# Optimization experiments

Hardware: AMD Instinct MI355X
Metric: run time of the kernel (lower is better)

Reference implementation:

```python
import jax, jax.numpy as jnp
import numpy as np

N_USER = 50000
N_ITEM = 50000
D_IN = 128
D_OUT = 128
N_EDGE = 600000


def _sage(x_src, x_dst, ei, Wl, bl, Wr):
    # PyG SAGEConv: out = lin_l(mean_{j in N(i)} x_j) + lin_r(x_i)
    # lin_l has bias, lin_r has no bias. Weights are [out, in].
    src, dst = ei[0], ei[1]
    n_dst = x_dst.shape[0]
    msg = x_src[src]                                            # [E, D_in] gather
    agg = jax.ops.segment_sum(msg, dst, num_segments=n_dst)     # [N_dst, D_in]
    cnt = jax.ops.segment_sum(jnp.ones((ei.shape[1],), x_src.dtype), dst,
                              num_segments=n_dst)
    mean = agg / jnp.maximum(cnt, 1.0)[:, None]                 # isolated nodes -> 0
    return mean @ Wl.T + bl + x_dst @ Wr.T


def setup_inputs() -> dict:
    key = jax.random.key(0)
    ks = jax.random.split(key, 16)
    inp = {
        "x_user": jax.random.normal(ks[0], (N_USER, D_IN), jnp.float32),
        "x_item": jax.random.normal(ks[1], (N_ITEM, D_IN), jnp.float32),
        "ei_rates": jax.random.randint(ks[2], (2, N_EDGE), 0, N_USER, jnp.int64 if jax.config.jax_enable_x64 else jnp.int32),
        "ei_rev": jax.random.randint(ks[3], (2, N_EDGE), 0, N_USER, jnp.int64 if jax.config.jax_enable_x64 else jnp.int32),
        "ei_follows": jax.random.randint(ks[4], (2, N_EDGE), 0, N_USER, jnp.int64 if jax.config.jax_enable_x64 else jnp.int32),
    }
    s = 1.0 / np.sqrt(D_IN)
    names = ["rates", "rev", "fol"]
    for i, nm in enumerate(names):
        inp[f"Wl_{nm}"] = jax.random.uniform(ks[5 + 3 * i], (D_OUT, D_IN), jnp.float32, -s, s)
        inp[f"bl_{nm}"] = jax.random.uniform(ks[6 + 3 * i], (D_OUT,), jnp.float32, -s, s)
        inp[f"Wr_{nm}"] = jax.random.uniform(ks[7 + 3 * i], (D_OUT, D_IN), jnp.float32, -s, s)
    return inp


def reference(x_user, x_item, ei_rates, ei_rev, ei_follows,
              Wl_rates, bl_rates, Wr_rates,
              Wl_rev, bl_rev, Wr_rev,
              Wl_fol, bl_fol, Wr_fol):
    # relation (user -rates-> item): src=user, dst=item
    out_item = _sage(x_user, x_item, ei_rates, Wl_rates, bl_rates, Wr_rates)
    # relation (item -rev_rates-> user): src=item, dst=user
    out_user_rev = _sage(x_item, x_user, ei_rev, Wl_rev, bl_rev, Wr_rev)
    # relation (user -follows-> user)
    out_user_fol = _sage(x_user, x_user, ei_follows, Wl_fol, bl_fol, Wr_fol)
    # HeteroConv aggr='mean': average relation outputs per dst node type
    out_user = (out_user_rev + out_user_fol) * 0.5
    return out_user, out_item
```

## Files before the change

### kernel.cpp

```cpp
#include <hip/hip_runtime.h>

#define D 128
#define NBB 392

typedef __attribute__((ext_vector_type(8))) short bf16x8;
typedef __attribute__((ext_vector_type(4))) float f32x4;

__device__ inline unsigned short f2bf(float f) {
  unsigned u = __builtin_bit_cast(unsigned, f);
  unsigned r = u + 0x7FFFu + ((u >> 16) & 1u);
  return (unsigned short)(r >> 16);
}
__device__ inline float bf2f(unsigned short b) {
  unsigned u = ((unsigned)b) << 16;
  return __builtin_bit_cast(float, u);
}

struct SetupArgs {
  const float* xu; const float* xi;
  unsigned short* xbu; unsigned short* xbi;
  int n4u, n4i, nbConv;
  const int* ei[3]; int ne[3]; int nbh[3]; int nbHist;
  int* bh;
  const float* Wl_rates; const float* Wr_rates; const float* bl_rates;
  const float* Wl_rev;   const float* Wr_rev;   const float* bl_rev;
  const float* Wl_fol;   const float* Wr_fol;   const float* bl_fol;
  unsigned short* Wb_user; unsigned short* Wb_item;
  float* b_user; float* b_item;
};

__global__ void __launch_bounds__(256) setup_kernel(SetupArgs S) {
  const int tid = threadIdx.x;
  int b = blockIdx.x;
  if (b < S.nbConv) {
    int i = b * 256 + tid;
    const float* x;
    unsigned short* xb;
    if (i < S.n4u) { x = S.xu; xb = S.xbu; }
    else { i -= S.n4u; if (i >= S.n4i) return; x = S.xi; xb = S.xbi; }
    float4 v = ((const float4*)x)[i];
    ushort4 o;
    o.x = f2bf(v.x); o.y = f2bf(v.y); o.z = f2bf(v.z); o.w = f2bf(v.w);
    ((ushort4*)xb)[i] = o;
    return;
  }
  b -= S.nbConv;
  if (b < S.nbHist) {
    int rel = 0;
    while (b >= S.nbh[rel]) { b -= S.nbh[rel]; rel++; }
    __shared__ int lh[NBB];
    for (int t = tid; t < NBB; t += 256) lh[t] = 0;
    __syncthreads();
    const int ne = S.ne[rel];
    const int* dsts = S.ei[rel] + ne;
    const int base = b * 2048;
#pragma unroll
    for (int k = 0; k < 8; k++) {
      int i = base + k * 256 + tid;
      if (i < ne) atomicAdd(&lh[dsts[i] >> 7], 1);
    }
    __syncthreads();
    for (int t = tid; t < NBB; t += 256)
      if (lh[t]) atomicAdd(&S.bh[rel * NBB + t], lh[t]);
    return;
  }
  b -= S.nbHist;
  int idx = b * 256 + tid;
  if (idx >= 128 * 384) return;
  int n = idx / 384, k = idx - n * 384;
  float v;
  if (k < 128)      v = 0.5f * S.Wl_rev[n * 128 + k];
  else if (k < 256) v = 0.5f * S.Wl_fol[n * 128 + (k - 128)];
  else              v = 0.5f * (S.Wr_rev[n * 128 + (k - 256)] + S.Wr_fol[n * 128 + (k - 256)]);
  S.Wb_user[n * 384 + k] = f2bf(v);
  if (k < 256) {
    float w = (k < 128) ? S.Wl_rates[n * 128 + k] : S.Wr_rates[n * 128 + (k - 128)];
    S.Wb_item[n * 256 + k] = f2bf(w);
  }
  if (idx < 128) {
    S.b_item[idx] = S.bl_rates[idx];
    S.b_user[idx] = 0.5f * (S.bl_rev[idx] + S.bl_fol[idx]);
  }
}

__global__ void __launch_bounds__(192) scanb_kernel(const int* __restrict__ bh,
                                                    int* __restrict__ bbase,
                                                    int* __restrict__ bcur, int nbkt) {
  int w = threadIdx.x >> 6, l = threadIdx.x & 63;
  if (w >= 3) return;
  const int off = w * NBB;
  int v[7];
  int s0 = 0;
#pragma unroll
  for (int k = 0; k < 7; k++) {
    int idx = l * 7 + k;
    v[k] = (idx < nbkt) ? bh[off + idx] : 0;
    s0 += v[k];
  }
  int s = s0;
  for (int dlt = 1; dlt < 64; dlt <<= 1) {
    int t = __shfl_up(s, dlt);
    if (l >= dlt) s += t;
  }
  int run = s - s0;
#pragma unroll
  for (int k = 0; k < 7; k++) {
    int idx = l * 7 + k;
    if (idx < nbkt) { bbase[off + idx] = run; bcur[off + idx] = run; run += v[k]; }
  }
  if (l == 63) bbase[off + nbkt] = run;
}

struct PArgs { const int* ei[3]; int ne[3]; int nb[3]; unsigned* part[3]; };

__global__ void __launch_bounds__(256) part_kernel(PArgs P, int* __restrict__ bcur,
                                                   int nbkt) {
  int b = blockIdx.x, rel = 0;
  while (b >= P.nb[rel]) { b -= P.nb[rel]; rel++; }
  const int ne = P.ne[rel];
  const int* src = P.ei[rel];
  const int* dst = src + ne;
  const int base = b * 4096;
  const int tn = min(4096, ne - base);
  __shared__ int lh[NBB], lscan[NBB], gb[NBB], lcur[NBB];
  __shared__ uint2 pairs[4096];
  const int tid = threadIdx.x;
  for (int t = tid; t < NBB; t += 256) lh[t] = 0;
  __syncthreads();
#pragma unroll
  for (int k = 0; k < 16; k++) {
    int i = base + k * 256 + tid;
    if (i < ne) atomicAdd(&lh[dst[i] >> 7], 1);
  }
  __syncthreads();
  if (tid < 64) {
    int v[7];
    int s0 = 0;
#pragma unroll
    for (int k = 0; k < 7; k++) {
      int idx = tid * 7 + k;
      v[k] = (idx < NBB) ? lh[idx] : 0;
      s0 += v[k];
    }
    int s = s0;
    for (int dlt = 1; dlt < 64; dlt <<= 1) {
      int t = __shfl_up(s, dlt);
      if (tid >= dlt) s += t;
    }
    int run = s - s0;
#pragma unroll
    for (int k = 0; k < 7; k++) {
      int idx = tid * 7 + k;
      if (idx < NBB) { lscan[idx] = run; run += v[k]; }
    }
  }
  __syncthreads();
  for (int t = tid; t < nbkt; t += 256) {
    gb[t] = atomicAdd(&bcur[rel * NBB + t], lh[t]);
    lcur[t] = lscan[t];
  }
  __syncthreads();
#pragma unroll
  for (int k = 0; k < 16; k++) {
    int i = base + k * 256 + tid;
    if (i < ne) {
      int d = dst[i];
      int slot = atomicAdd(&lcur[d >> 7], 1);
      pairs[slot] = (uint2){(unsigned)src[i], (unsigned)d};
    }
  }
  __syncthreads();
  unsigned* __restrict__ out = P.part[rel];
#pragma unroll
  for (int k = 0; k < 16; k++) {
    int slot = k * 256 + tid;
    if (slot < tn) {
      uint2 p = pairs[slot];
      int bin = (int)(p.y >> 7);
      out[gb[bin] + (slot - lscan[bin])] = p.x | ((p.y & 127u) << 25);
    }
  }
}

struct BAArgs {
  const unsigned* part[3];
  const unsigned short* xb[3];
  unsigned short* mean[3];
  int m[3];
};

__global__ void __launch_bounds__(256) bagg_kernel(BAArgs A, const int* __restrict__ bbase,
                                                   int nbkt) {
  const int rel = blockIdx.x / nbkt;
  const int b = blockIdx.x - rel * nbkt;
  const int bs = bbase[rel * NBB + b];
  const int be = bbase[rel * NBB + b + 1];
  const int n = be - bs;
  const unsigned* __restrict__ pp = A.part[rel] + bs;
  const unsigned short* __restrict__ x = A.xb[rel];
  unsigned short* __restrict__ mean = A.mean[rel];
  const int m = A.m[rel];
  const int tid = threadIdx.x;
  const int w = tid >> 6, lane = tid & 63;
  const size_t loff = lane * 2;
  __shared__ unsigned sorted[4096];
  __shared__ int lcnt[128], lofs[128], lcur[128];

  if (n > 4096) {
    for (int r = w; r < 128; r += 4) {
      int gdst = b * 128 + r;
      if (gdst >= m) break;
      float a0 = 0.f, a1 = 0.f;
      int cnt = 0;
      for (int j = 0; j < n; j++) {
        unsigned p = pp[j];
        if ((int)(p >> 25) == r) {
          unsigned v = *(const unsigned*)(x + (size_t)(p & 0x1FFFFFFu) * D + loff);
          a0 += bf2f((unsigned short)(v & 0xFFFFu));
          a1 += bf2f((unsigned short)(v >> 16));
          cnt++;
        }
      }
      float inv = 1.0f / (float)max(cnt, 1);
      unsigned o = (unsigned)f2bf(a0 * inv) | ((unsigned)f2bf(a1 * inv) << 16);
      *(unsigned*)(mean + (size_t)gdst * D + loff) = o;
    }
    return;
  }

  if (tid < 128) lcnt[tid] = 0;
  __syncthreads();
  for (int i = tid; i < n; i += 256) atomicAdd(&lcnt[pp[i] >> 25], 1);
  __syncthreads();
  if (tid < 64) {
    int v0 = lcnt[2 * tid], v1 = lcnt[2 * tid + 1];
    int s0 = v0 + v1, s = s0;
    for (int dlt = 1; dlt < 64; dlt <<= 1) {
      int t = __shfl_up(s, dlt);
      if (tid >= dlt) s += t;
    }
    int ex = s - s0;
    lofs[2 * tid] = ex;
    lofs[2 * tid + 1] = ex + v0;
  }
  __syncthreads();
  if (tid < 128) lcur[tid] = lofs[tid];
  __syncthreads();
  for (int i = tid; i < n; i += 256) {
    unsigned p = pp[i];
    int slot = atomicAdd(&lcur[p >> 25], 1);
    sorted[slot] = p & 0x1FFFFFFu;
  }
  __syncthreads();

  for (int r = w; r < 128; r += 8) {
    const int rA = r, rB = r + 4;
    const int gA = b * 128 + rA, gB = b * 128 + rB;
    if (gA >= m) break;
    const bool doB = gB < m;
    int jA = lofs[rA];
    const int eA = lcur[rA];
    int jB = doB ? lofs[rB] : 0;
    const int eB = doB ? lcur[rB] : 0;
    float aA0=0,aA1=0,bA0=0,bA1=0,cA0=0,cA1=0,dA0=0,dA1=0;
    float aB0=0,aB1=0,bB0=0,bB1=0,cB0=0,cB1=0,dB0=0,dB1=0;
    while (jA + 4 <= eA && jB + 4 <= eB) {
      unsigned sA0 = sorted[jA], sA1 = sorted[jA+1], sA2 = sorted[jA+2], sA3 = sorted[jA+3];
      unsigned sB0 = sorted[jB], sB1 = sorted[jB+1], sB2 = sorted[jB+2], sB3 = sorted[jB+3];
      unsigned vA0 = *(const unsigned*)(x + (size_t)sA0 * D + loff);
      unsigned vA1 = *(const unsigned*)(x + (size_t)sA1 * D + loff);
      unsigned vA2 = *(const unsigned*)(x + (size_t)sA2 * D + loff);
      unsigned vA3 = *(const unsigned*)(x + (size_t)sA3 * D + loff);
      unsigned vB0 = *(const unsigned*)(x + (size_t)sB0 * D + loff);
      unsigned vB1 = *(const unsigned*)(x + (size_t)sB1 * D + loff);
      unsigned vB2 = *(const unsigned*)(x + (size_t)sB2 * D + loff);
      unsigned vB3 = *(const unsigned*)(x + (size_t)sB3 * D + loff);
      aA0 += bf2f((unsigned short)(vA0 & 0xFFFFu)); aA1 += bf2f((unsigned short)(vA0 >> 16));
      bA0 += bf2f((unsigned short)(vA1 & 0xFFFFu)); bA1 += bf2f((unsigned short)(vA1 >> 16));
      cA0 += bf2f((unsigned short)(vA2 & 0xFFFFu)); cA1 += bf2f((unsigned short)(vA2 >> 16));
      dA0 += bf2f((unsigned short)(vA3 & 0xFFFFu)); dA1 += bf2f((unsigned short)(vA3 >> 16));
      aB0 += bf2f((unsigned short)(vB0 & 0xFFFFu)); aB1 += bf2f((unsigned short)(vB0 >> 16));
      bB0 += bf2f((unsigned short)(vB1 & 0xFFFFu)); bB1 += bf2f((unsigned short)(vB1 >> 16));
      cB0 += bf2f((unsigned short)(vB2 & 0xFFFFu)); cB1 += bf2f((unsigned short)(vB2 >> 16));
      dB0 += bf2f((unsigned short)(vB3 & 0xFFFFu)); dB1 += bf2f((unsigned short)(vB3 >> 16));
      jA += 4; jB += 4;
    }
    for (; jA + 4 <= eA; jA += 4) {
      unsigned s0 = sorted[jA], s1 = sorted[jA+1], s2 = sorted[jA+2], s3 = sorted[jA+3];
      unsigned v0 = *(const unsigned*)(x + (size_t)s0 * D + loff);
      unsigned v1 = *(const unsigned*)(x + (size_t)s1 * D + loff);
      unsigned v2 = *(const unsigned*)(x + (size_t)s2 * D + loff);
      unsigned v3 = *(const unsigned*)(x + (size_t)s3 * D + loff);
      aA0 += bf2f((unsigned short)(v0 & 0xFFFFu)); aA1 += bf2f((unsigned short)(v0 >> 16));
      bA0 += bf2f((unsigned short)(v1 & 0xFFFFu)); bA1 += bf2f((unsigned short)(v1 >> 16));
      cA0 += bf2f((unsigned short)(v2 & 0xFFFFu)); cA1 += bf2f((unsigned short)(v2 >> 16));
      dA0 += bf2f((unsigned short)(v3 & 0xFFFFu)); dA1 += bf2f((unsigned short)(v3 >> 16));
    }
    for (; jA < eA; jA++) {
      unsigned s = sorted[jA];
      unsigned v = *(const unsigned*)(x + (size_t)s * D + loff);
      aA0 += bf2f((unsigned short)(v & 0xFFFFu)); aA1 += bf2f((unsigned short)(v >> 16));
    }
    for (; jB + 4 <= eB; jB += 4) {
      unsigned s0 = sorted[jB], s1 = sorted[jB+1], s2 = sorted[jB+2], s3 = sorted[jB+3];
      unsigned v0 = *(const unsigned*)(x + (size_t)s0 * D + loff);
      unsigned v1 = *(const unsigned*)(x + (size_t)s1 * D + loff);
      unsigned v2 = *(const unsigned*)(x + (size_t)s2 * D + loff);
      unsigned v3 = *(const unsigned*)(x + (size_t)s3 * D + loff);
      aB0 += bf2f((unsigned short)(v0 & 0xFFFFu)); aB1 += bf2f((unsigned short)(v0 >> 16));
      bB0 += bf2f((unsigned short)(v1 & 0xFFFFu)); bB1 += bf2f((unsigned short)(v1 >> 16));
      cB0 += bf2f((unsigned short)(v2 & 0xFFFFu)); cB1 += bf2f((unsigned short)(v2 >> 16));
      dB0 += bf2f((unsigned short)(v3 & 0xFFFFu)); dB1 += bf2f((unsigned short)(v3 >> 16));
    }
    for (; jB < eB; jB++) {
      unsigned s = sorted[jB];
      unsigned v = *(const unsigned*)(x + (size_t)s * D + loff);
      aB0 += bf2f((unsigned short)(v & 0xFFFFu)); aB1 += bf2f((unsigned short)(v >> 16));
    }
    {
      float v0 = (aA0 + bA0) + (cA0 + dA0);
      float v1 = (aA1 + bA1) + (cA1 + dA1);
      float inv = 1.0f / (float)max(eA - lofs[rA], 1);
      unsigned o = (unsigned)f2bf(v0 * inv) | ((unsigned)f2bf(v1 * inv) << 16);
      *(unsigned*)(mean + (size_t)gA * D + loff) = o;
    }
    if (doB) {
      float v0 = (aB0 + bB0) + (cB0 + dB0);
      float v1 = (aB1 + bB1) + (cB1 + dB1);
      float inv = 1.0f / (float)max(eB - lofs[rB], 1);
      unsigned o = (unsigned)f2bf(v0 * inv) | ((unsigned)f2bf(v1 * inv) << 16);
      *(unsigned*)(mean + (size_t)gB * D + loff) = o;
    }
  }
}

struct BSrcs { const unsigned short* s[3]; };
struct GemmArgs {
  BSrcs su, si;
  const unsigned short* wbU; const unsigned short* wbI;
  const float* bU; const float* bI;
  float* outU; float* outI;
  int MU, MI, nbU;
};

__global__ void __launch_bounds__(256) gemm2_kernel(GemmArgs A) {
  const bool isU = (int)blockIdx.x < A.nbU;
  const int bid = isU ? blockIdx.x : blockIdx.x - A.nbU;
  const BSrcs S = isU ? A.su : A.si;
  const unsigned short* __restrict__ Wb = isU ? A.wbU : A.wbI;
  const int K = isU ? 384 : 256;
  const float* __restrict__ bias = isU ? A.bU : A.bI;
  float* __restrict__ out = isU ? A.outU : A.outI;
  const int M = isU ? A.MU : A.MI;

  __shared__ __align__(16) unsigned short As[128][72];
  __shared__ __align__(16) unsigned short Ws[128][72];
  const int tid = threadIdx.x;
  const int lane = tid & 63;
  const int wave = tid >> 6;
  const int wr = (wave >> 1) * 64;
  const int wc = (wave & 1) * 64;
  const int l15 = lane & 15;
  const int quad = lane >> 4;
  const int m0 = bid * 128;

  f32x4 acc[4][4];
#pragma unroll
  for (int r = 0; r < 4; r++)
#pragma unroll
    for (int c = 0; c < 4; c++) acc[r][c] = (f32x4){0.f, 0.f, 0.f, 0.f};

  const int srow = tid >> 1, shalf = tid & 1;
  const int nchunks = K >> 6;
  for (int ch = 0; ch < nchunks; ch++) {
    const unsigned short* sp = S.s[ch >> 1];
    const int coff = (ch & 1) << 6;
    {
      int mm = min(m0 + srow, M - 1);
      const uint4* g = (const uint4*)(sp + (size_t)mm * D + coff + shalf * 32);
      uint4* ld = (uint4*)(&As[srow][shalf * 32]);
      ld[0] = g[0]; ld[1] = g[1]; ld[2] = g[2]; ld[3] = g[3];
    }
    {
      const uint4* g = (const uint4*)(Wb + (size_t)srow * K + ch * 64 + shalf * 32);
      uint4* ld = (uint4*)(&Ws[srow][shalf * 32]);
      ld[0] = g[0]; ld[1] = g[1]; ld[2] = g[2]; ld[3] = g[3];
    }
    __syncthreads();
#pragma unroll
    for (int kk = 0; kk < 64; kk += 32) {
      const int kb = kk + quad * 8;
      bf16x8 a0 = *(const bf16x8*)&As[wr + l15][kb];
      bf16x8 a1 = *(const bf16x8*)&As[wr + 16 + l15][kb];
      bf16x8 a2 = *(const bf16x8*)&As[wr + 32 + l15][kb];
      bf16x8 a3 = *(const bf16x8*)&As[wr + 48 + l15][kb];
      bf16x8 b0 = *(const bf16x8*)&Ws[wc + l15][kb];
      bf16x8 b1 = *(const bf16x8*)&Ws[wc + 16 + l15][kb];
      bf16x8 b2 = *(const bf16x8*)&Ws[wc + 32 + l15][kb];
      bf16x8 b3 = *(const bf16x8*)&Ws[wc + 48 + l15][kb];
      acc[0][0] = __builtin_amdgcn_mfma_f32_16x16x32_bf16(a0, b0, acc[0][0], 0, 0, 0);
      acc[0][1] = __builtin_amdgcn_mfma_f32_16x16x32_bf16(a0, b1, acc[0][1], 0, 0, 0);
      acc[0][2] = __builtin_amdgcn_mfma_f32_16x16x32_bf16(a0, b2, acc[0][2], 0, 0, 0);
      acc[0][3] = __builtin_amdgcn_mfma_f32_16x16x32_bf16(a0, b3, acc[0][3], 0, 0, 0);
      acc[1][0] = __builtin_amdgcn_mfma_f32_16x16x32_bf16(a1, b0, acc[1][0], 0, 0, 0);
      acc[1][1] = __builtin_amdgcn_mfma_f32_16x16x32_bf16(a1, b1, acc[1][1], 0, 0, 0);
      acc[1][2] = __builtin_amdgcn_mfma_f32_16x16x32_bf16(a1, b2, acc[1][2], 0, 0, 0);
      acc[1][3] = __builtin_amdgcn_mfma_f32_16x16x32_bf16(a1, b3, acc[1][3], 0, 0, 0);
      acc[2][0] = __builtin_amdgcn_mfma_f32_16x16x32_bf16(a2, b0, acc[2][0], 0, 0, 0);
      acc[2][1] = __builtin_amdgcn_mfma_f32_16x16x32_bf16(a2, b1, acc[2][1], 0, 0, 0);
      acc[2][2] = __builtin_amdgcn_mfma_f32_16x16x32_bf16(a2, b2, acc[2][2], 0, 0, 0);
      acc[2][3] = __builtin_amdgcn_mfma_f32_16x16x32_bf16(a2, b3, acc[2][3], 0, 0, 0);
      acc[3][0] = __builtin_amdgcn_mfma_f32_16x16x32_bf16(a3, b0, acc[3][0], 0, 0, 0);
      acc[3][1] = __builtin_amdgcn_mfma_f32_16x16x32_bf16(a3, b1, acc[3][1], 0, 0, 0);
      acc[3][2] = __builtin_amdgcn_mfma_f32_16x16x32_bf16(a3, b2, acc[3][2], 0, 0, 0);
      acc[3][3] = __builtin_amdgcn_mfma_f32_16x16x32_bf16(a3, b3, acc[3][3], 0, 0, 0);
    }
    __syncthreads();
  }
#pragma unroll
  for (int c = 0; c < 4; c++) {
    const int n = wc + c * 16 + l15;
    const float bv = bias[n];
#pragma unroll
    for (int r = 0; r < 4; r++) {
      const int mrow = m0 + wr + r * 16 + quad * 4;
#pragma unroll
      for (int i = 0; i < 4; i++) {
        if (mrow + i < M) out[(size_t)(mrow + i) * D + n] = acc[r][c][i] + bv;
      }
    }
  }
}

extern "C" void kernel_launch(void* const* d_in, const int* in_sizes, int n_in,
                              void* d_out, int out_size, void* d_ws, size_t ws_size,
                              hipStream_t stream) {
  const float* x_user   = (const float*)d_in[0];
  const float* x_item   = (const float*)d_in[1];
  const int*   ei_rates = (const int*)d_in[2];
  const int*   ei_rev   = (const int*)d_in[3];
  const int*   ei_fol   = (const int*)d_in[4];
  const float* Wl_rates = (const float*)d_in[5];
  const float* bl_rates = (const float*)d_in[6];
  const float* Wr_rates = (const float*)d_in[7];
  const float* Wl_rev   = (const float*)d_in[8];
  const float* bl_rev   = (const float*)d_in[9];
  const float* Wr_rev   = (const float*)d_in[10];
  const float* Wl_fol   = (const float*)d_in[11];
  const float* bl_fol   = (const float*)d_in[12];
  const float* Wr_fol   = (const float*)d_in[13];

  const int NU = in_sizes[0] / D;
  const int NI = in_sizes[1] / D;
  const int E_rates = in_sizes[2] / 2;
  const int E_rev   = in_sizes[3] / 2;
  const int E_fol   = in_sizes[4] / 2;
  const int nbkt = ((NU > NI ? NU : NI) + 127) / 128;

  char* wsb = (char*)d_ws;
  size_t off = 0;
  auto take = [&](size_t bytes) {
    char* p = wsb + off;
    off += (bytes + 15) & ~(size_t)15;
    return p;
  };
  int* bhist = (int*)take(3 * NBB * 4);
  const size_t zero_bytes = off;
  int* bbase = (int*)take(3 * NBB * 4);
  int* bcur  = (int*)take(3 * NBB * 4);
  unsigned* part_rates = (unsigned*)take((size_t)E_rates * 4);
  unsigned* part_rev   = (unsigned*)take((size_t)E_rev * 4);
  unsigned* part_fol   = (unsigned*)take((size_t)E_fol * 4);
  unsigned short* xb_user    = (unsigned short*)take((size_t)NU * D * 2);
  unsigned short* xb_item    = (unsigned short*)take((size_t)NI * D * 2);
  unsigned short* mean_rates = (unsigned short*)take((size_t)NI * D * 2);
  unsigned short* mean_rev   = (unsigned short*)take((size_t)NU * D * 2);
  unsigned short* mean_fol   = (unsigned short*)take((size_t)NU * D * 2);
  unsigned short* Wb_user    = (unsigned short*)take(128 * 384 * 2);
  unsigned short* Wb_item    = (unsigned short*)take(128 * 256 * 2);
  float* b_user = (float*)take(128 * 4);
  float* b_item = (float*)take(128 * 4);

  hipMemsetAsync(d_ws, 0, zero_bytes, stream);

  SetupArgs SA;
  SA.xu = x_user; SA.xi = x_item; SA.xbu = xb_user; SA.xbi = xb_item;
  SA.n4u = NU * D / 4; SA.n4i = NI * D / 4;
  SA.nbConv = (SA.n4u + SA.n4i + 255) / 256;
  SA.ei[0] = ei_rates; SA.ne[0] = E_rates; SA.nbh[0] = (E_rates + 2047) / 2048;
  SA.ei[1] = ei_rev;   SA.ne[1] = E_rev;   SA.nbh[1] = (E_rev + 2047) / 2048;
  SA.ei[2] = ei_fol;   SA.ne[2] = E_fol;   SA.nbh[2] = (E_fol + 2047) / 2048;
  SA.nbHist = SA.nbh[0] + SA.nbh[1] + SA.nbh[2];
  SA.bh = bhist;
  SA.Wl_rates = Wl_rates; SA.Wr_rates = Wr_rates; SA.bl_rates = bl_rates;
  SA.Wl_rev = Wl_rev; SA.Wr_rev = Wr_rev; SA.bl_rev = bl_rev;
  SA.Wl_fol = Wl_fol; SA.Wr_fol = Wr_fol; SA.bl_fol = bl_fol;
  SA.Wb_user = Wb_user; SA.Wb_item = Wb_item;
  SA.b_user = b_user; SA.b_item = b_item;
  const int nbPrep = (128 * 384 + 255) / 256;
  setup_kernel<<<SA.nbConv + SA.nbHist + nbPrep, 256, 0, stream>>>(SA);

  scanb_kernel<<<1, 192, 0, stream>>>(bhist, bbase, bcur, nbkt);

  PArgs P;
  P.ei[0] = ei_rates; P.ne[0] = E_rates; P.nb[0] = (E_rates + 4095) / 4096; P.part[0] = part_rates;
  P.ei[1] = ei_rev;   P.ne[1] = E_rev;   P.nb[1] = (E_rev + 4095) / 4096;   P.part[1] = part_rev;
  P.ei[2] = ei_fol;   P.ne[2] = E_fol;   P.nb[2] = (E_fol + 4095) / 4096;   P.part[2] = part_fol;
  part_kernel<<<P.nb[0] + P.nb[1] + P.nb[2], 256, 0, stream>>>(P, bcur, nbkt);

  BAArgs BA;
  BA.part[0] = part_rates; BA.xb[0] = xb_user; BA.mean[0] = mean_rates; BA.m[0] = NI;
  BA.part[1] = part_rev;   BA.xb[1] = xb_item; BA.mean[1] = mean_rev;   BA.m[1] = NU;
  BA.part[2] = part_fol;   BA.xb[2] = xb_user; BA.mean[2] = mean_fol;   BA.m[2] = NU;
  bagg_kernel<<<3 * nbkt, 256, 0, stream>>>(BA, bbase, nbkt);

  GemmArgs gma;
  gma.su.s[0] = mean_rev;   gma.su.s[1] = mean_fol; gma.su.s[2] = xb_user;
  gma.si.s[0] = mean_rates; gma.si.s[1] = xb_item;  gma.si.s[2] = nullptr;
  gma.wbU = Wb_user; gma.wbI = Wb_item;
  gma.bU = b_user;   gma.bI = b_item;
  gma.outU = (float*)d_out;
  gma.outI = (float*)d_out + (size_t)NU * D;
  gma.MU = NU; gma.MI = NI;
  gma.nbU = (NU + 127) / 128;
  const int nbI = (NI + 127) / 128;
  gemm2_kernel<<<gma.nbU + nbI, 256, 0, stream>>>(gma);
}
```

Baseline: 308.1 us.

## Fuse bucketed neighbor-mean aggregation into the GEMM kernel via shared memory

Merges the bucket aggregation kernel into the MFMA GEMM kernel. Each 128-row block computes the per-relation mean directly into a shared-memory A tile and multiplies it against the matching weight slice, so the bf16 mean buffers are never written to or read back from global memory and one launch disappears. It also skips the global atomicAdd in partitioning for empty bins. The trade-off is fewer independent blocks doing gather work (user blocks now handle two relations serially), larger shared-memory use that may lower occupancy, and gather latency that is no longer overlapped with MFMA work in other blocks.

After: 350.9 us. 1.14x slower.

```diff
diff --git a/kernel.cpp b/kernel.cpp
--- a/kernel.cpp
+++ b/kernel.cpp
@@ -156,7 +156,8 @@
   }
   __syncthreads();
   for (int t = tid; t < nbkt; t += 256) {
-    gb[t] = atomicAdd(&bcur[rel * NBB + t], lh[t]);
+    int c = lh[t];
+    gb[t] = c ? atomicAdd(&bcur[rel * NBB + t], c) : 0;
     lcur[t] = lscan[t];
   }
   __syncthreads();
@@ -182,187 +183,41 @@
   }
 }
 
-struct BAArgs {
+struct FArgs {
   const unsigned* part[3];
-  const unsigned short* xb[3];
-  unsigned short* mean[3];
-  int m[3];
-};
-
-__global__ void __launch_bounds__(256) bagg_kernel(BAArgs A, const int* __restrict__ bbase,
-                                                   int nbkt) {
-  const int rel = blockIdx.x / nbkt;
-  const int b = blockIdx.x - rel * nbkt;
-  const int bs = bbase[rel * NBB + b];
-  const int be = bbase[rel * NBB + b + 1];
-  const int n = be - bs;
-  const unsigned* __restrict__ pp = A.part[rel] + bs;
-  const unsigned short* __restrict__ x = A.xb[rel];
-  unsigned short* __restrict__ mean = A.mean[rel];
-  const int m = A.m[rel];
-  const int tid = threadIdx.x;
-  const int w = tid >> 6, lane = tid & 63;
-  const size_t loff = lane * 2;
-  __shared__ unsigned sorted[4096];
-  __shared__ int lcnt[128], lofs[128], lcur[128];
-
-  if (n > 4096) {
-    for (int r = w; r < 128; r += 4) {
-      int gdst = b * 128 + r;
-      if (gdst >= m) break;
-      float a0 = 0.f, a1 = 0.f;
-      int cnt = 0;
-      for (int j = 0; j < n; j++) {
-        unsigned p = pp[j];
-        if ((int)(p >> 25) == r) {
-          unsigned v = *(const unsigned*)(x + (size_t)(p & 0x1FFFFFFu) * D + loff);
-          a0 += bf2f((unsigned short)(v & 0xFFFFu));
-          a1 += bf2f((unsigned short)(v >> 16));
-          cnt++;
-        }
-      }
-      float inv = 1.0f / (float)max(cnt, 1);
-      unsigned o = (unsigned)f2bf(a0 * inv) | ((unsigned)f2bf(a1 * inv) << 16);
-      *(unsigned*)(mean + (size_t)gdst * D + loff) = o;
-    }
-    return;
-  }
-
-  if (tid < 128) lcnt[tid] = 0;
-  __syncthreads();
-  for (int i = tid; i < n; i += 256) atomicAdd(&lcnt[pp[i] >> 25], 1);
-  __syncthreads();
-  if (tid < 64) {
-    int v0 = lcnt[2 * tid], v1 = lcnt[2 * tid + 1];
-    int s0 = v0 + v1, s = s0;
-    for (int dlt = 1; dlt < 64; dlt <<= 1) {
-      int t = __shfl_up(s, dlt);
-      if (tid >= dlt) s += t;
-    }
-    int ex = s - s0;
-    lofs[2 * tid] = ex;
-    lofs[2 * tid + 1] = ex + v0;
-  }
-  __syncthreads();
-  if (tid < 128) lcur[tid] = lofs[tid];
-  __syncthreads();
-  for (int i = tid; i < n; i += 256) {
-    unsigned p = pp[i];
-    int slot = atomicAdd(&lcur[p >> 25], 1);
-    sorted[slot] = p & 0x1FFFFFFu;
-  }
-  __syncthreads();
-
-  for (int r = w; r < 128; r += 8) {
-    const int rA = r, rB = r + 4;
-    const int gA = b * 128 + rA, gB = b * 128 + rB;
-    if (gA >= m) break;
-    const bool doB = gB < m;
-    int jA = lofs[rA];
-    const int eA = lcur[rA];
-    int jB = doB ? lofs[rB] : 0;
-    const int eB = doB ? lcur[rB] : 0;
-    float aA0=0,aA1=0,bA0=0,bA1=0,cA0=0,cA1=0,dA0=0,dA1=0;
-    float aB0=0,aB1=0,bB0=0,bB1=0,cB0=0,cB1=0,dB0=0,dB1=0;
-    while (jA + 4 <= eA && jB + 4 <= eB) {
-      unsigned sA0 = sorted[jA], sA1 = sorted[jA+1], sA2 = sorted[jA+2], sA3 = sorted[jA+3];
-      unsigned sB0 = sorted[jB], sB1 = sorted[jB+1], sB2 = sorted[jB+2], sB3 = sorted[jB+3];
-      unsigned vA0 = *(const unsigned*)(x + (size_t)sA0 * D + loff);
-      unsigned vA1 = *(const unsigned*)(x + (size_t)sA1 * D + loff);
-      unsigned vA2 = *(const unsigned*)(x + (size_t)sA2 * D + loff);
-      unsigned vA3 = *(const unsigned*)(x + (size_t)sA3 * D + loff);
-      unsigned vB0 = *(const unsigned*)(x + (size_t)sB0 * D + loff);
-      unsigned vB1 = *(const unsigned*)(x + (size_t)sB1 * D + loff);
-      unsigned vB2 = *(const unsigned*)(x + (size_t)sB2 * D + loff);
-      unsigned vB3 = *(const unsigned*)(x + (size_t)sB3 * D + loff);
-      aA0 += bf2f((unsigned short)(vA0 & 0xFFFFu)); aA1 += bf2f((unsigned short)(vA0 >> 16));
-      bA0 += bf2f((unsigned short)(vA1 & 0xFFFFu)); bA1 += bf2f((unsigned short)(vA1 >> 16));
-      cA0 += bf2f((unsigned short)(vA2 & 0xFFFFu)); cA1 += bf2f((unsigned short)(vA2 >> 16));
-      dA0 += bf2f((unsigned short)(vA3 & 0xFFFFu)); dA1 += bf2f((unsigned short)(vA3 >> 16));
-      aB0 += bf2f((unsigned short)(vB0 & 0xFFFFu)); aB1 += bf2f((unsigned short)(vB0 >> 16));
-      bB0 += bf2f((unsigned short)(vB1 & 0xFFFFu)); bB1 += bf2f((unsigned short)(vB1 >> 16));
-      cB0 += bf2f((unsigned short)(vB2 & 0xFFFFu)); cB1 += bf2f((unsigned short)(vB2 >> 16));
-      dB0 += bf2f((unsigned short)(vB3 & 0xFFFFu)); dB1 += bf2f((unsigned short)(vB3 >> 16));
-      jA += 4; jB += 4;
-    }
-    for (; jA + 4 <= eA; jA += 4) {
-      unsigned s0 = sorted[jA], s1 = sorted[jA+1], s2 = sorted[jA+2], s3 = sorted[jA+3];
-      unsigned v0 = *(const unsigned*)(x + (size_t)s0 * D + loff);
-      unsigned v1 = *(const unsigned*)(x + (size_t)s1 * D + loff);
-      unsigned v2 = *(const unsigned*)(x + (size_t)s2 * D + loff);
-      unsigned v3 = *(const unsigned*)(x + (size_t)s3 * D + loff);
-      aA0 += bf2f((unsigned short)(v0 & 0xFFFFu)); aA1 += bf2f((unsigned short)(v0 >> 16));
-      bA0 += bf2f((unsigned short)(v1 & 0xFFFFu)); bA1 += bf2f((unsigned short)(v1 >> 16));
-      cA0 += bf2f((unsigned short)(v2 & 0xFFFFu)); cA1 += bf2f((unsigned short)(v2 >> 16));
-      dA0 += bf2f((unsigned short)(v3 & 0xFFFFu)); dA1 += bf2f((unsigned short)(v3 >> 16));
-    }
-    for (; jA < eA; jA++) {
-      unsigned s = sorted[jA];
-      unsigned v = *(const unsigned*)(x + (size_t)s * D + loff);
-      aA0 += bf2f((unsigned short)(v & 0xFFFFu)); aA1 += bf2f((unsigned short)(v >> 16));
-    }
-    for (; jB + 4 <= eB; jB += 4) {
-      unsigned s0 = sorted[jB], s1 = sorted[jB+1], s2 = sorted[jB+2], s3 = sorted[jB+3];
-      unsigned v0 = *(const unsigned*)(x + (size_t)s0 * D + loff);
-      unsigned v1 = *(const unsigned*)(x + (size_t)s1 * D + loff);
-      unsigned v2 = *(const unsigned*)(x + (size_t)s2 * D + loff);
-      unsigned v3 = *(const unsigned*)(x + (size_t)s3 * D + loff);
-      aB0 += bf2f((unsigned short)(v0 & 0xFFFFu)); aB1 += bf2f((unsigned short)(v0 >> 16));
-      bB0 += bf2f((unsigned short)(v1 & 0xFFFFu)); bB1 += bf2f((unsigned short)(v1 >> 16));
-      cB0 += bf2f((unsigned short)(v2 & 0xFFFFu)); cB1 += bf2f((unsigned short)(v2 >> 16));
-      dB0 += bf2f((unsigned short)(v3 & 0xFFFFu)); dB1 += bf2f((unsigned short)(v3 >> 16));
-    }
-    for (; jB < eB; jB++) {
-      unsigned s = sorted[jB];
-      unsigned v = *(const unsigned*)(x + (size_t)s * D + loff);
-      aB0 += bf2f((unsigned short)(v & 0xFFFFu)); aB1 += bf2f((unsigned short)(v >> 16));
-    }
-    {
-      float v0 = (aA0 + bA0) + (cA0 + dA0);
-      float v1 = (aA1 + bA1) + (cA1 + dA1);
-      float inv = 1.0f / (float)max(eA - lofs[rA], 1);
-      unsigned o = (unsigned)f2bf(v0 * inv) | ((unsigned)f2bf(v1 * inv) << 16);
-      *(unsigned*)(mean + (size_t)gA * D + loff) = o;
-    }
-    if (doB) {
-      float v0 = (aB0 + bB0) + (cB0 + dB0);
-      float v1 = (aB1 + bB1) + (cB1 + dB1);
-      float inv = 1.0f / (float)max(eB - lofs[rB], 1);
-      unsigned o = (unsigned)f2bf(v0 * inv) | ((unsigned)f2bf(v1 * inv) << 16);
-      *(unsigned*)(mean + (size_t)gB * D + loff) = o;
-    }
-  }
-}
-
-struct BSrcs { const unsigned short* s[3]; };
-struct GemmArgs {
-  BSrcs su, si;
+  const unsigned short* gxb[3];
+  const unsigned short* xbU; const unsigned short* xbI;
   const unsigned short* wbU; const unsigned short* wbI;
   const float* bU; const float* bI;
   float* outU; float* outI;
   int MU, MI, nbU;
 };
 
-__global__ void __launch_bounds__(256) gemm2_kernel(GemmArgs A) {
+__global__ void __launch_bounds__(256) bg_kernel(FArgs A, const int* __restrict__ bbase,
+                                                 int nbkt) {
   const bool isU = (int)blockIdx.x < A.nbU;
-  const int bid = isU ? blockIdx.x : blockIdx.x - A.nbU;
-  const BSrcs S = isU ? A.su : A.si;
+  const int b = isU ? blockIdx.x : blockIdx.x - A.nbU;
+  const int m0 = b * 128;
+  const int M = isU ? A.MU : A.MI;
   const unsigned short* __restrict__ Wb = isU ? A.wbU : A.wbI;
   const int K = isU ? 384 : 256;
   const float* __restrict__ bias = isU ? A.bU : A.bI;
   float* __restrict__ out = isU ? A.outU : A.outI;
-  const int M = isU ? A.MU : A.MI;
-
-  __shared__ __align__(16) unsigned short As[128][72];
+  const int nparts = isU ? 3 : 2;
+
+  __shared__ __align__(16) unsigned short As[128][136];
   __shared__ __align__(16) unsigned short Ws[128][72];
+  __shared__ unsigned sorted[4096];
+  __shared__ int lcnt[128], lofs[128], lcur[128];
+
   const int tid = threadIdx.x;
   const int lane = tid & 63;
-  const int wave = tid >> 6;
-  const int wr = (wave >> 1) * 64;
-  const int wc = (wave & 1) * 64;
+  const int w = tid >> 6;
+  const int wr = (w >> 1) * 64;
+  const int wc = (w & 1) * 64;
   const int l15 = lane & 15;
   const int quad = lane >> 4;
-  const int m0 = bid * 128;
+  const size_t loff = (size_t)lane * 2;
 
   f32x4 acc[4][4];
 #pragma unroll
@@ -370,53 +225,189 @@
 #pragma unroll
     for (int c = 0; c < 4; c++) acc[r][c] = (f32x4){0.f, 0.f, 0.f, 0.f};
 
-  const int srow = tid >> 1, shalf = tid & 1;
-  const int nchunks = K >> 6;
-  for (int ch = 0; ch < nchunks; ch++) {
-    const unsigned short* sp = S.s[ch >> 1];
-    const int coff = (ch & 1) << 6;
-    {
+  for (int p = 0; p < nparts; p++) {
+    const bool isX = (p == nparts - 1);
+    if (isX) {
+      const unsigned short* xsrc = isU ? A.xbU : A.xbI;
+      const int srow = tid >> 1, shalf = tid & 1;
       int mm = min(m0 + srow, M - 1);
-      const uint4* g = (const uint4*)(sp + (size_t)mm * D + coff + shalf * 32);
-      uint4* ld = (uint4*)(&As[srow][shalf * 32]);
-      ld[0] = g[0]; ld[1] = g[1]; ld[2] = g[2]; ld[3] = g[3];
-    }
-    {
-      const uint4* g = (const uint4*)(Wb + (size_t)srow * K + ch * 64 + shalf * 32);
-      uint4* ld = (uint4*)(&Ws[srow][shalf * 32]);
-      ld[0] = g[0]; ld[1] = g[1]; ld[2] = g[2]; ld[3] = g[3];
+      const uint4* g = (const uint4*)(xsrc + (size_t)mm * D + shalf * 64);
+      uint4* ld = (uint4*)(&As[srow][shalf * 64]);
+#pragma unroll
+      for (int q = 0; q < 8; q++) ld[q] = g[q];
+    } else {
+      const int rel = isU ? (p + 1) : 0;
+      const int bs = bbase[rel * NBB + b];
+      const int be = bbase[rel * NBB + b + 1];
+      const int n = be - bs;
+      const unsigned* __restrict__ pp = A.part[rel] + bs;
+      const unsigned short* __restrict__ x = A.gxb[rel];
+
+      if (n > 4096) {
+        for (int r = w; r < 128; r += 4) {
+          float a0 = 0.f, a1 = 0.f;
+          int cnt = 0;
+          for (int j = 0; j < n; j++) {
+            unsigned pk = pp[j];
+            if ((int)(pk >> 25) == r) {
+              unsigned v = *(const unsigned*)(x + (size_t)(pk & 0x1FFFFFFu) * D + loff);
+              a0 += bf2f((unsigned short)(v & 0xFFFFu));
+              a1 += bf2f((unsigned short)(v >> 16));
+              cnt++;
+            }
+          }
+          float inv = 1.0f / (float)max(cnt, 1);
+          unsigned o = (unsigned)f2bf(a0 * inv) | ((unsigned)f2bf(a1 * inv) << 16);
+          *(unsigned*)(&As[r][2 * lane]) = o;
+        }
+      } else {
+        if (tid < 128) lcnt[tid] = 0;
+        __syncthreads();
+        for (int i = tid; i < n; i += 256) atomicAdd(&lcnt[pp[i] >> 25], 1);
+        __syncthreads();
+        if (tid < 64) {
+          int v0 = lcnt[2 * tid], v1 = lcnt[2 * tid + 1];
+          int s0 = v0 + v1, s = s0;
+          for (int dlt = 1; dlt < 64; dlt <<= 1) {
+            int t = __shfl_up(s, dlt);
+            if (tid >= dlt) s += t;
+          }
+          int ex = s - s0;
+          lofs[2 * tid] = ex;
+          lofs[2 * tid + 1] = ex + v0;
+        }
+        __syncthreads();
+        if (tid < 128) lcur[tid] = lofs[tid];
+        __syncthreads();
+        for (int i = tid; i < n; i += 256) {
+          unsigned pk = pp[i];
+          int slot = atomicAdd(&lcur[pk >> 25], 1);
+          sorted[slot] = pk & 0x1FFFFFFu;
+        }
+        __syncthreads();
+
+        for (int r = w; r < 128; r += 8) {
+          const int rA = r, rB = r + 4;
+          int jA = lofs[rA];
+          const int eA = lcur[rA];
+          int jB = lofs[rB];
+          const int eB = lcur[rB];
+          float aA0=0,aA1=0,bA0=0,bA1=0,cA0=0,cA1=0,dA0=0,dA1=0;
+          float aB0=0,aB1=0,bB0=0,bB1=0,cB0=0,cB1=0,dB0=0,dB1=0;
+          while (jA + 4 <= eA && jB + 4 <= eB) {
+            unsigned sA0 = sorted[jA], sA1 = sorted[jA+1], sA2 = sorted[jA+2], sA3 = sorted[jA+3];
+            unsigned sB0 = sorted[jB], sB1 = sorted[jB+1], sB2 = sorted[jB+2], sB3 = sorted[jB+3];
+            unsigned vA0 = *(const unsigned*)(x + (size_t)sA0 * D + loff);
+            unsigned vA1 = *(const unsigned*)(x + (size_t)sA1 * D + loff);
+            unsigned vA2 = *(const unsigned*)(x + (size_t)sA2 * D + loff);
+            unsigned vA3 = *(const unsigned*)(x + (size_t)sA3 * D + loff);
+            unsigned vB0 = *(const unsigned*)(x + (size_t)sB0 * D + loff);
+            unsigned vB1 = *(const unsigned*)(x + (size_t)sB1 * D + loff);
+            unsigned vB2 = *(const unsigned*)(x + (size_t)sB2 * D + loff);
+            unsigned vB3 = *(const unsigned*)(x + (size_t)sB3 * D + loff);
+            aA0 += bf2f((unsigned short)(vA0 & 0xFFFFu)); aA1 += bf2f((unsigned short)(vA0 >> 16));
+            bA0 += bf2f((unsigned short)(vA1 & 0xFFFFu)); bA1 += bf2f((unsigned short)(vA1 >> 16));
+            cA0 += bf2f((unsigned short)(vA2 & 0xFFFFu)); cA1 += bf2f((unsigned short)(vA2 >> 16));
+            dA0 += bf2f((unsigned short)(vA3 & 0xFFFFu)); dA1 += bf2f((unsigned short)(vA3 >> 16));
+            aB0 += bf2f((unsigned short)(vB0 & 0xFFFFu)); aB1 += bf2f((unsigned short)(vB0 >> 16));
+            bB0 += bf2f((unsigned short)(vB1 & 0xFFFFu)); bB1 += bf2f((unsigned short)(vB1 >> 16));
+            cB0 += bf2f((unsigned short)(vB2 & 0xFFFFu)); cB1 += bf2f((unsigned short)(vB2 >> 16));
+            dB0 += bf2f((unsigned short)(vB3 & 0xFFFFu)); dB1 += bf2f((unsigned short)(vB3 >> 16));
+            jA += 4; jB += 4;
+          }
+          for (; jA + 4 <= eA; jA += 4) {
+            unsigned s0 = sorted[jA], s1 = sorted[jA+1], s2 = sorted[jA+2], s3 = sorted[jA+3];
+            unsigned v0 = *(const unsigned*)(x + (size_t)s0 * D + loff);
+            unsigned v1 = *(const unsigned*)(x + (size_t)s1 * D + loff);
+            unsigned v2 = *(const unsigned*)(x + (size_t)s2 * D + loff);
+            unsigned v3 = *(const unsigned*)(x + (size_t)s3 * D + loff);
+            aA0 += bf2f((unsigned short)(v0 & 0xFFFFu)); aA1 += bf2f((unsigned short)(v0 >> 16));
+            bA0 += bf2f((unsigned short)(v1 & 0xFFFFu)); bA1 += bf2f((unsigned short)(v1 >> 16));
+            cA0 += bf2f((unsigned short)(v2 & 0xFFFFu)); cA1 += bf2f((unsigned short)(v2 >> 16));
+            dA0 += bf2f((unsigned short)(v3 & 0xFFFFu)); dA1 += bf2f((unsigned short)(v3 >> 16));
+          }
+          for (; jA < eA; jA++) {
+            unsigned s = sorted[jA];
+            unsigned v = *(const unsigned*)(x + (size_t)s * D + loff);
+            aA0 += bf2f((unsigned short)(v & 0xFFFFu)); aA1 += bf2f((unsigned short)(v >> 16));
+          }
+          for (; jB + 4 <= eB; jB += 4) {
+            unsigned s0 = sorted[jB], s1 = sorted[jB+1], s2 = sorted[jB+2], s3 = sorted[jB+3];
+            unsigned v0 = *(const unsigned*)(x + (size_t)s0 * D + loff);
+            unsigned v1 = *(const unsigned*)(x + (size_t)s1 * D + loff);
+            unsigned v2 = *(const unsigned*)(x + (size_t)s2 * D + loff);
+            unsigned v3 = *(const unsigned*)(x + (size_t)s3 * D + loff);
+            aB0 += bf2f((unsigned short)(v0 & 0xFFFFu)); aB1 += bf2f((unsigned short)(v0 >> 16));
+            bB0 += bf2f((unsigned short)(v1 & 0xFFFFu)); bB1 += bf2f((unsigned short)(v1 >> 16));
+            cB0 += bf2f((unsigned short)(v2 & 0xFFFFu)); cB1 += bf2f((unsigned short)(v2 >> 16));
+            dB0 += bf2f((unsigned short)(v3 & 0xFFFFu)); dB1 += bf2f((unsigned short)(v3 >> 16));
+          }
+          for (; jB < eB; jB++) {
+            unsigned s = sorted[jB];
+            unsigned v = *(const unsigned*)(x + (size_t)s * D + loff);
+            aB0 += bf2f((unsigned short)(v & 0xFFFFu)); aB1 += bf2f((unsigned short)(v >> 16));
+          }
+          {
+            float v0 = (aA0 + bA0) + (cA0 + dA0);
+            float v1 = (aA1 + bA1) + (cA1 + dA1);
+            float inv = 1.0f / (float)max(eA - lofs[rA], 1);
+            unsigned o = (unsigned)f2bf(v0 * inv) | ((unsigned)f2bf(v1 * inv) << 16);
+            *(unsigned*)(&As[rA][2 * lane]) = o;
+          }
+          {
+            float v0 = (aB0 + bB0) + (cB0 + dB0);
+            float v1 = (aB1 + bB1) + (cB1 + dB1);
+            float inv = 1.0f / (float)max(eB - lofs[rB], 1);
+            unsigned o = (unsigned)f2bf(v0 * inv) | ((unsigned)f2bf(v1 * inv) << 16);
+            *(unsigned*)(&As[rB][2 * lane]) = o;
+          }
+        }
+      }
     }
     __syncthreads();
-#pragma unroll
-    for (int kk = 0; kk < 64; kk += 32) {
-      const int kb = kk + quad * 8;
-      bf16x8 a0 = *(const bf16x8*)&As[wr + l15][kb];
-      bf16x8 a1 = *(const bf16x8*)&As[wr + 16 + l15][kb];
-      bf16x8 a2 = *(const bf16x8*)&As[wr + 32 + l15][kb];
-      bf16x8 a3 = *(const bf16x8*)&As[wr + 48 + l15][kb];
-      bf16x8 b0 = *(const bf16x8*)&Ws[wc + l15][kb];
-      bf16x8 b1 = *(const bf16x8*)&Ws[wc + 16 + l15][kb];
-      bf16x8 b2 = *(const bf16x8*)&Ws[wc + 32 + l15][kb];
-      bf16x8 b3 = *(const bf16x8*)&Ws[wc + 48 + l15][kb];
-      acc[0][0] = __builtin_amdgcn_mfma_f32_16x16x32_bf16(a0, b0, acc[0][0], 0, 0, 0);
-      acc[0][1] = __builtin_amdgcn_mfma_f32_16x16x32_bf16(a0, b1, acc[0][1], 0, 0, 0);
-      acc[0][2] = __builtin_amdgcn_mfma_f32_16x16x32_bf16(a0, b2, acc[0][2], 0, 0, 0);
-      acc[0][3] = __builtin_amdgcn_mfma_f32_16x16x32_bf16(a0, b3, acc[0][3], 0, 0, 0);
-      acc[1][0] = __builtin_amdgcn_mfma_f32_16x16x32_bf16(a1, b0, acc[1][0], 0, 0, 0);
-      acc[1][1] = __builtin_amdgcn_mfma_f32_16x16x32_bf16(a1, b1, acc[1][1], 0, 0, 0);
-      acc[1][2] = __builtin_amdgcn_mfma_f32_16x16x32_bf16(a1, b2, acc[1][2], 0, 0, 0);
-      acc[1][3] = __builtin_amdgcn_mfma_f32_16x16x32_bf16(a1, b3, acc[1][3], 0, 0, 0);
-      acc[2][0] = __builtin_amdgcn_mfma_f32_16x16x32_bf16(a2, b0, acc[2][0], 0, 0, 0);
-      acc[2][1] = __builtin_amdgcn_mfma_f32_16x16x32_bf16(a2, b1, acc[2][1], 0, 0, 0);
-      acc[2][2] = __builtin_amdgcn_mfma_f32_16x16x32_bf16(a2, b2, acc[2][2], 0, 0, 0);
-      acc[2][3] = __builtin_amdgcn_mfma_f32_16x16x32_bf16(a2, b3, acc[2][3], 0, 0, 0);
-      acc[3][0] = __builtin_amdgcn_mfma_f32_16x16x32_bf16(a3, b0, acc[3][0], 0, 0, 0);
-      acc[3][1] = __builtin_amdgcn_mfma_f32_16x16x32_bf16(a3, b1, acc[3][1], 0, 0, 0);
-      acc[3][2] = __builtin_amdgcn_mfma_f32_16x16x32_bf16(a3, b2, acc[3][2], 0, 0, 0);
-      acc[3][3] = __builtin_amdgcn_mfma_f32_16x16x32_bf16(a3, b3, acc[3][3], 0, 0, 0);
-    }
-    __syncthreads();
-  }
+
+#pragma unroll
+    for (int ch = 0; ch < 2; ch++) {
+      {
+        const int srow = tid >> 1, shalf = tid & 1;
+        const uint4* g = (const uint4*)(Wb + (size_t)srow * K + p * 128 + ch * 64 + shalf * 32);
+        uint4* ld = (uint4*)(&Ws[srow][shalf * 32]);
+        ld[0] = g[0]; ld[1] = g[1]; ld[2] = g[2]; ld[3] = g[3];
+      }
+      __syncthreads();
+#pragma unroll
+      for (int kk = 0; kk < 64; kk += 32) {
+        const int ab = ch * 64 + kk + quad * 8;
+        const int kb = kk + quad * 8;
+        bf16x8 a0 = *(const bf16x8*)&As[wr + l15][ab];
+        bf16x8 a1 = *(const bf16x8*)&As[wr + 16 + l15][ab];
+        bf16x8 a2 = *(const bf16x8*)&As[wr + 32 + l15][ab];
+        bf16x8 a3 = *(const bf16x8*)&As[wr + 48 + l15][ab];
+        bf16x8 b0 = *(const bf16x8*)&Ws[wc + l15][kb];
+        bf16x8 b1 = *(const bf16x8*)&Ws[wc + 16 + l15][kb];
+        bf16x8 b2 = *(const bf16x8*)&Ws[wc + 32 + l15][kb];
+        bf16x8 b3 = *(const bf16x8*)&Ws[wc + 48 + l15][kb];
+        acc[0][0] = __builtin_amdgcn_mfma_f32_16x16x32_bf16(a0, b0, acc[0][0], 0, 0, 0);
+        acc[0][1] = __builtin_amdgcn_mfma_f32_16x16x32_bf16(a0, b1, acc[0][1], 0, 0, 0);
+        acc[0][2] = __builtin_amdgcn_mfma_f32_16x16x32_bf16(a0, b2, acc[0][2], 0, 0, 0);
+        acc[0][3] = __builtin_amdgcn_mfma_f32_16x16x32_bf16(a0, b3, acc[0][3], 0, 0, 0);
+        acc[1][0] = __builtin_amdgcn_mfma_f32_16x16x32_bf16(a1, b0, acc[1][0], 0, 0, 0);
+        acc[1][1] = __builtin_amdgcn_mfma_f32_16x16x32_bf16(a1, b1, acc[1][1], 0, 0, 0);
+        acc[1][2] = __builtin_amdgcn_mfma_f32_16x16x32_bf16(a1, b2, acc[1][2], 0, 0, 0);
+        acc[1][3] = __builtin_amdgcn_mfma_f32_16x16x32_bf16(a1, b3, acc[1][3], 0, 0, 0);
+        acc[2][0] = __builtin_amdgcn_mfma_f32_16x16x32_bf16(a2, b0, acc[2][0], 0, 0, 0);
+        acc[2][1] = __builtin_amdgcn_mfma_f32_16x16x32_bf16(a2, b1, acc[2][1], 0, 0, 0);
+        acc[2][2] = __builtin_amdgcn_mfma_f32_16x16x32_bf16(a2, b2, acc[2][2], 0, 0, 0);
+        acc[2][3] = __builtin_amdgcn_mfma_f32_16x16x32_bf16(a2, b3, acc[2][3], 0, 0, 0);
+        acc[3][0] = __builtin_amdgcn_mfma_f32_16x16x32_bf16(a3, b0, acc[3][0], 0, 0, 0);
+        acc[3][1] = __builtin_amdgcn_mfma_f32_16x16x32_bf16(a3, b1, acc[3][1], 0, 0, 0);
+        acc[3][2] = __builtin_amdgcn_mfma_f32_16x16x32_bf16(a3, b2, acc[3][2], 0, 0, 0);
+        acc[3][3] = __builtin_amdgcn_mfma_f32_16x16x32_bf16(a3, b3, acc[3][3], 0, 0, 0);
+      }
+      __syncthreads();
+    }
+  }
+
 #pragma unroll
   for (int c = 0; c < 4; c++) {
     const int n = wc + c * 16 + l15;
@@ -471,13 +462,10 @@
   unsigned* part_rates = (unsigned*)take((size_t)E_rates * 4);
   unsigned* part_rev   = (unsigned*)take((size_t)E_rev * 4);
   unsigned* part_fol   = (unsigned*)take((size_t)E_fol * 4);
-  unsigned short* xb_user    = (unsigned short*)take((size_t)NU * D * 2);
-  unsigned short* xb_item    = (unsigned short*)take((size_t)NI * D * 2);
-  unsigned short* mean_rates = (unsigned short*)take((size_t)NI * D * 2);
-  unsigned short* mean_rev   = (unsigned short*)take((size_t)NU * D * 2);
-  unsigned short* mean_fol   = (unsigned short*)take((size_t)NU * D * 2);
-  unsigned short* Wb_user    = (unsigned short*)take(128 * 384 * 2);
-  unsigned short* Wb_item    = (unsigned short*)take(128 * 256 * 2);
+  unsigned short* xb_user = (unsigned short*)take((size_t)NU * D * 2);
+  unsigned short* xb_item = (unsigned short*)take((size_t)NI * D * 2);
+  unsigned short* Wb_user = (unsigned short*)take(128 * 384 * 2);
+  unsigned short* Wb_item = (unsigned short*)take(128 * 256 * 2);
   float* b_user = (float*)take(128 * 4);
   float* b_item = (float*)take(128 * 4);
 
@@ -508,21 +496,17 @@
   P.ei[2] = ei_fol;   P.ne[2] = E_fol;   P.nb[2] = (E_fol + 4095) / 4096;   P.part[2] = part_fol;
   part_kernel<<<P.nb[0] + P.nb[1] + P.nb[2], 256, 0, stream>>>(P, bcur, nbkt);
 
-  BAArgs BA;
-  BA.part[0] = part_rates; BA.xb[0] = xb_user; BA.mean[0] = mean_rates; BA.m[0] = NI;
-  BA.part[1] = part_rev;   BA.xb[1] = xb_item; BA.mean[1] = mean_rev;   BA.m[1] = NU;
-  BA.part[2] = part_fol;   BA.xb[2] = xb_user; BA.mean[2] = mean_fol;   BA.m[2] = NU;
-  bagg_kernel<<<3 * nbkt, 256, 0, stream>>>(BA, bbase, nbkt);
-
-  GemmArgs gma;
-  gma.su.s[0] = mean_rev;   gma.su.s[1] = mean_fol; gma.su.s[2] = xb_user;
-  gma.si.s[0] = mean_rates; gma.si.s[1] = xb_item;  gma.si.s[2] = nullptr;
-  gma.wbU = Wb_user; gma.wbI = Wb_item;
-  gma.bU = b_user;   gma.bI = b_item;
-  gma.outU = (float*)d_out;
-  gma.outI = (float*)d_out + (size_t)NU * D;
-  gma.MU = NU; gma.MI = NI;
-  gma.nbU = (NU + 127) / 128;
+  FArgs FA;
+  FA.part[0] = part_rates; FA.gxb[0] = xb_user;
+  FA.part[1] = part_rev;   FA.gxb[1] = xb_item;
+  FA.part[2] = part_fol;   FA.gxb[2] = xb_user;
+  FA.xbU = xb_user; FA.xbI = xb_item;
+  FA.wbU = Wb_user; FA.wbI = Wb_item;
+  FA.bU = b_user;   FA.bI = b_item;
+  FA.outU = (float*)d_out;
+  FA.outI = (float*)d_out + (size_t)NU * D;
+  FA.MU = NU; FA.MI = NI;
+  FA.nbU = (NU + 127) / 128;
   const int nbI = (NI + 127) / 128;
-  gemm2_kernel<<<gma.nbU + nbI, 256, 0, stream>>>(gma);
-}
+  bg_kernel<<<FA.nbU + nbI, 256, 0, stream>>>(FA, bbase, nbkt);
+}
```
